# Kernel tuning notes

Hardware: AMD Instinct MI355X
Metric: run time of the kernel (lower is better)

## Reference

```python
import jax, jax.numpy as jnp
import numpy as np

BLK = 46  # hardcoded block size in the original module
EPS = 1e-5


def setup_inputs() -> dict:
    key = jax.random.key(0)
    ks = jax.random.split(key, 13)
    N, C, Ci = 128, 512, 256
    return {
        "ori_feature": jax.random.normal(ks[0], (N, C, BLK), jnp.float32),
        "bn_gamma": jax.random.uniform(ks[1], (C,), jnp.float32),
        "bn_beta": jax.random.normal(ks[2], (C,), jnp.float32),
        "bn_mean": jax.random.normal(ks[3], (C,), jnp.float32),
        "bn_var": jax.random.uniform(ks[4], (C,), jnp.float32),
        "theta_w": jax.random.normal(ks[5], (Ci, C), jnp.float32) * 0.02,
        "theta_b": jax.random.normal(ks[6], (Ci,), jnp.float32) * 0.02,
        "phi_w": jax.random.normal(ks[7], (Ci, C), jnp.float32) * 0.02,
        "phi_b": jax.random.normal(ks[8], (Ci,), jnp.float32) * 0.02,
        "g_w": jax.random.normal(ks[9], (Ci, C), jnp.float32) * 0.02,
        "g_b": jax.random.normal(ks[10], (Ci,), jnp.float32) * 0.02,
        "W_w": jax.random.normal(ks[11], (C, Ci), jnp.float32) * 0.02,
        "W_b": jax.random.normal(ks[12], (C,), jnp.float32) * 0.02,
    }


def reference(ori_feature, bn_gamma, bn_beta, bn_mean, bn_var,
              theta_w, theta_b, phi_w, phi_b, g_w, g_b, W_w, W_b):
    N, C, num = ori_feature.shape  # (N, C, 46)
    # BatchNorm1d (inference-style, per-channel) + ReLU
    inv = bn_gamma / jnp.sqrt(bn_var + EPS)
    feat = jax.nn.relu(ori_feature * inv[None, :, None]
                       + (bn_beta - bn_mean * inv)[None, :, None])
    feat = feat.transpose(0, 2, 1).reshape(N * num, C)  # (T, C)
    x_theta = feat @ theta_w.T + theta_b  # (T, Ci)
    x_phi = feat @ phi_w.T + phi_b        # (T, Ci)
    attn = x_theta @ x_phi.T              # (T, T)
    # block-diagonal masking: entries within the same 46-token block set to -1000
    blk = jnp.arange(N * num) // num
    attn = jnp.where(blk[:, None] == blk[None, :], jnp.float32(-1000.0), attn)
    f_div_C = jax.nn.softmax(attn, axis=-1)
    g_x = feat @ g_w.T + g_b              # (T, Ci)
    y = f_div_C @ g_x                     # (T, Ci)
    W_y = (y @ W_w.T + W_b).reshape(N, num, C)
    att_fea = ori_feature.transpose(0, 2, 1) + W_y  # (N, 46, C)
    return att_fea, f_div_C
```

## Files before the change

kernel.cpp:

```cpp
#include <hip/hip_runtime.h>
#include <math.h>

#define N_BATCH 128
#define C_DIM   512
#define BLKSZ   46
#define T_DIM   (N_BATCH * BLKSZ)
#define CI      256
#define EPS_BN  1e-5f
#define NCB     (T_DIM / 128)

typedef __attribute__((ext_vector_type(8))) short bf16x8;
typedef __attribute__((ext_vector_type(4))) float f32x4;

__device__ __forceinline__ short f2bf(float f) {
    union { float f; unsigned u; } v; v.f = f;
    unsigned r = v.u + 0x7fffu + ((v.u >> 16) & 1u);
    return (short)(r >> 16);
}

__device__ __forceinline__ float h2f(unsigned short h) {
    _Float16 x; __builtin_memcpy(&x, &h, 2); return (float)x;
}
__device__ __forceinline__ unsigned short f2h(float f) {
    _Float16 x = (_Float16)f; unsigned short u; __builtin_memcpy(&u, &x, 2); return u;
}

__device__ __forceinline__ void gload16(const void* g, void* l) {
    __builtin_amdgcn_global_load_lds((__attribute__((address_space(1))) void*)g,
                                     (__attribute__((address_space(3))) void*)l,
                                     16, 0, 0);
}

template <int A> struct avec_sel { using t = float4; };
template <> struct avec_sel<2> { using t = ushort4; };

__global__ __launch_bounds__(256) void bn_relu_kernel(
    const float* __restrict__ ori, const float* __restrict__ gamma,
    const float* __restrict__ beta, const float* __restrict__ mean,
    const float* __restrict__ var, short* __restrict__ feat)
{
    __shared__ short tile[256 * BLKSZ];
    const int n = blockIdx.y;
    const int c0 = blockIdx.x * 256;
    const int tid = threadIdx.x;
    for (int i = tid; i < 256 * BLKSZ; i += 256) {
        int cl = i / BLKSZ, b = i - cl * BLKSZ;
        int c = c0 + cl;
        float inv = gamma[c] * rsqrtf(var[c] + EPS_BN);
        float v = ori[((size_t)n * C_DIM + c) * BLKSZ + b] * inv + (beta[c] - mean[c] * inv);
        tile[cl * BLKSZ + b] = f2bf(fmaxf(v, 0.0f));
    }
    __syncthreads();
    for (int i = tid; i < BLKSZ * 256; i += 256) {
        int b = i >> 8, cl = i & 255;
        feat[(size_t)(n * BLKSZ + b) * C_DIM + c0 + cl] = tile[cl * BLKSZ + b];
    }
}

__global__ __launch_bounds__(256) void cvt_kernel(
    const float* __restrict__ thw, const float* __restrict__ phw,
    const float* __restrict__ gw, const float* __restrict__ Ww,
    const float* __restrict__ thb, const float* __restrict__ phb,
    const float* __restrict__ gb,
    short* __restrict__ wall, short* __restrict__ wW, float* __restrict__ bcat)
{
    const int i = blockIdx.x * 256 + threadIdx.x;
    const float* src[4] = {thw, phw, gw, Ww};
    short* dst[4] = {wall, wall + 256 * 512, wall + 512 * 512, wW};
    #pragma unroll
    for (int m = 0; m < 4; ++m) {
        float4 v = *(const float4*)(src[m] + (size_t)i * 4);
        short4 t = make_short4(f2bf(v.x), f2bf(v.y), f2bf(v.z), f2bf(v.w));
        *(short4*)(dst[m] + (size_t)i * 4) = t;
    }
    if (blockIdx.x == 0) {
        bcat[threadIdx.x] = thb[threadIdx.x];
        bcat[threadIdx.x + 256] = phb[threadIdx.x];
        bcat[threadIdx.x + 512] = gb[threadIdx.x];
    }
}

template <int EPI, int ACVT, int BM, int BN, int OCC = 2>
__global__ __launch_bounds__(256, OCC) void gemm_nt(
    const void* __restrict__ Avoid, const short* __restrict__ B,
    const float* __restrict__ bias, void* __restrict__ Cvoid,
    int M, int Nn, int K, int lda, int ldb, int nsplit,
    const float* __restrict__ ori,
    float* __restrict__ stats, const float* __restrict__ rowstat,
    float* __restrict__ fout)
{
    constexpr int NWC = BN / 64;
    constexpr int NWR = 4 / NWC;
    constexpr int MI  = BM / (NWR * 16);
    constexpr int NBUF = (ACVT != 0) ? 2 : 1;
    static_assert((EPI != 5 && EPI != 6 && EPI != 7) || NWC == 2, "stats/split epilogue assumes NWC==2");
    static_assert(ACVT == 0 || BN == 256, "pipelined vmcnt count assumes BN==256");
    __shared__ short As[NBUF * BM * 32];
    __shared__ short Bs[NBUF * BN * 32];
    const int tid = threadIdx.x;
    const int w = tid >> 6, lane = tid & 63;

    int bx = blockIdx.x, by = blockIdx.y;
    if constexpr (EPI == 5 || EPI == 6) {
        const int nwg = gridDim.x * gridDim.y;
        const int orig = by * gridDim.x + bx;
        const int q = nwg >> 3, r = nwg & 7;
        const int xcd = orig & 7, idx = orig >> 3;
        const int wg = (xcd < r ? xcd * (q + 1) : r * (q + 1) + (xcd - r) * q) + idx;
        bx = wg % gridDim.x; by = wg / gridDim.x;
    }
    const int m0 = by * BM, n0 = bx * BN;
    const int wr = w / NWC, wc = w % NWC;
    const int wrow = wr * (MI * 16);

    const int kper = K / 32 / nsplit;
    const int kt0 = blockIdx.z * kper, kt1 = kt0 + kper;

    f32x4 acc[MI][4] = {};

    const int sr = tid >> 2;
    const int sc = (tid & 3) * 8;
    const short* Ab = (const short*)Avoid;

    if constexpr (ACVT == 0) {
        for (int kt = kt0; kt < kt1; ++kt) {
            const int k0 = kt * 32;
            #pragma unroll
            for (int p = 0; p < BM / 64; ++p)
                gload16(Ab + (size_t)(m0 + p * 64 + sr) * lda + k0 + sc,
                        &As[(p * 64 + sr) * 32 + sc]);
            #pragma unroll
            for (int p = 0; p < BN / 64; ++p)
                gload16(B + (size_t)(n0 + p * 64 + sr) * ldb + k0 + sc,
                        &Bs[(p * 64 + sr) * 32 + sc]);
            __syncthreads();

            bf16x8 af[MI], bfr[4];
            #pragma unroll
            for (int i = 0; i < MI; ++i)
                af[i] = *(bf16x8*)&As[(wrow + i * 16 + (lane & 15)) * 32 + (lane >> 4) * 8];
            #pragma unroll
            for (int j = 0; j < 4; ++j)
                bfr[j] = *(bf16x8*)&Bs[(wc * 64 + j * 16 + (lane & 15)) * 32 + (lane >> 4) * 8];
            #pragma unroll
            for (int i = 0; i < MI; ++i)
                #pragma unroll
                for (int j = 0; j < 4; ++j)
                    acc[i][j] = __builtin_amdgcn_mfma_f32_16x16x32_bf16(af[i], bfr[j], acc[i][j], 0, 0, 0);
            __syncthreads();
        }
    } else {
        constexpr int EPT = BM * 32 / 256;
        static_assert(EPT == 4, "pipelined ACVT path assumes EPT==4");
        constexpr int TPR = 32 / EPT;
        const int a_r = tid / TPR;
        const int a_c = (tid % TPR) * EPT;
        float2 st = ((const float2*)rowstat)[m0 + a_r];
        const float rm = st.x, rz = st.y;
        using AV = typename avec_sel<ACVT>::t;
        const AV* Arow = (const AV*)((const char*)Avoid
                         + ((size_t)(m0 + a_r) * lda) * (ACVT == 2 ? 2 : 4));
        float* frow = fout + (size_t)(m0 + a_r) * lda;

        AV hv = Arow[(kt0 * 32 + a_c) / 4];
        #pragma unroll
        for (int p = 0; p < BN / 64; ++p)
            gload16(B + (size_t)(n0 + p * 64 + sr) * ldb + kt0 * 32 + sc,
                    &Bs[(p * 64 + sr) * 32 + sc]);

        for (int kt = kt0; kt < kt1; ++kt) {
            const int cur = (kt - kt0) & 1;
            const int kc = kt * 32 + a_c;
            float4 vf;
            if constexpr (ACVT == 2) {
                vf.x = h2f(hv.x); vf.y = h2f(hv.y); vf.z = h2f(hv.z); vf.w = h2f(hv.w);
            } else {
                vf.x = hv.x; vf.y = hv.y; vf.z = hv.z; vf.w = hv.w;
            }
            float4 e;
            e.x = expf(vf.x - rm) * rz; e.y = expf(vf.y - rm) * rz;
            e.z = expf(vf.z - rm) * rz; e.w = expf(vf.w - rm) * rz;
            *(float4*)(frow + kc) = e;
            short4 t = make_short4(f2bf(e.x), f2bf(e.y), f2bf(e.z), f2bf(e.w));
            *(short4*)&As[cur * BM * 32 + a_r * 32 + a_c] = t;

            if (kt + 1 < kt1) {
                hv = Arow[((kt + 1) * 32 + a_c) / 4];
                #pragma unroll
                for (int p = 0; p < BN / 64; ++p)
                    gload16(B + (size_t)(n0 + p * 64 + sr) * ldb + (kt + 1) * 32 + sc,
                            &Bs[(cur ^ 1) * BN * 32 + (p * 64 + sr) * 32 + sc]);
                asm volatile("s_waitcnt vmcnt(6) lgkmcnt(0)\n\ts_barrier" ::: "memory");
            } else {
                asm volatile("s_waitcnt vmcnt(1) lgkmcnt(0)\n\ts_barrier" ::: "memory");
            }

            bf16x8 af[MI], bfr[4];
            #pragma unroll
            for (int i = 0; i < MI; ++i)
                af[i] = *(bf16x8*)&As[cur * BM * 32 + (wrow + i * 16 + (lane & 15)) * 32 + (lane >> 4) * 8];
            #pragma unroll
            for (int j = 0; j < 4; ++j)
                bfr[j] = *(bf16x8*)&Bs[cur * BN * 32 + (wc * 64 + j * 16 + (lane & 15)) * 32 + (lane >> 4) * 8];
            #pragma unroll
            for (int i = 0; i < MI; ++i)
                #pragma unroll
                for (int j = 0; j < 4; ++j)
                    acc[i][j] = __builtin_amdgcn_mfma_f32_16x16x32_bf16(af[i], bfr[j], acc[i][j], 0, 0, 0);
            asm volatile("s_barrier" ::: "memory");
        }
    }

    const int col = lane & 15, rowq = lane >> 4;

    if constexpr (EPI == 5 || EPI == 6) {
        __shared__ float sm[NWC][BM];
        __shared__ float ss[NWC][BM];
        int cbj[4];
        #pragma unroll
        for (int j = 0; j < 4; ++j)
            cbj[j] = (n0 + wc * 64 + j * 16 + col) / BLKSZ;
        #pragma unroll
        for (int i = 0; i < MI; ++i) {
            #pragma unroll
            for (int r = 0; r < 4; ++r) {
                const int trow = wrow + i * 16 + rowq * 4 + r;
                const int grow = m0 + trow;
                const int rb = grow / BLKSZ;
                float vj[4];
                float vmax = -1e30f;
                #pragma unroll
                for (int j = 0; j < 4; ++j) {
                    float v = acc[i][j][r];
                    if (cbj[j] == rb) v = -30000.0f;
                    const size_t idx = (size_t)grow * Nn + (n0 + wc * 64 + j * 16 + col);
                    if constexpr (EPI == 6) {
                        unsigned short hh = f2h(v);
                        ((unsigned short*)Cvoid)[idx] = hh;
                        v = h2f(hh);
                    } else {
                        ((float*)Cvoid)[idx] = v;
                    }
                    vj[j] = v;
                    vmax = fmaxf(vmax, v);
                }
                #pragma unroll
                for (int off = 1; off < 16; off <<= 1)
                    vmax = fmaxf(vmax, __shfl_xor(vmax, off));
                float s = 0.f;
                #pragma unroll
                for (int j = 0; j < 4; ++j) s += expf(vj[j] - vmax);
                #pragma unroll
                for (int off = 1; off < 16; off <<= 1)
                    s += __shfl_xor(s, off);
                if (col == 0) { sm[wc][trow] = vmax; ss[wc][trow] = s; }
            }
        }
        __syncthreads();
        if (tid < BM) {
            const float ma = sm[0][tid], mb = sm[1][tid];
            const float mx = fmaxf(ma, mb);
            const float S = ss[0][tid] * expf(ma - mx) + ss[1][tid] * expf(mb - mx);
            ((float2*)stats)[(size_t)bx * M + (m0 + tid)] = make_float2(mx, S);
        }
    } else if constexpr (EPI == 7) {
        if (n0 < 512) {
            #pragma unroll
            for (int i = 0; i < MI; ++i)
                #pragma unroll
                for (int j = 0; j < 4; ++j)
                    #pragma unroll
                    for (int r = 0; r < 4; ++r) {
                        const int grow = m0 + wrow + i * 16 + rowq * 4 + r;
                        const int gcol = n0 + wc * 64 + j * 16 + col;
                        ((short*)Cvoid)[(size_t)grow * 512 + gcol] =
                            f2bf(acc[i][j][r] + bias[gcol]);
                    }
        } else {
            short* gxTp = (short*)stats;
            #pragma unroll
            for (int i = 0; i < MI; ++i)
                #pragma unroll
                for (int j = 0; j < 4; ++j) {
                    const int grow0 = m0 + wrow + i * 16 + rowq * 4;
                    const int gcol = n0 + wc * 64 + j * 16 + col;
                    const float bv = bias[gcol];
                    short4 t = make_short4(
                        f2bf(acc[i][j][0] + bv), f2bf(acc[i][j][1] + bv),
                        f2bf(acc[i][j][2] + bv), f2bf(acc[i][j][3] + bv));
                    *(short4*)&gxTp[(size_t)(gcol - 512) * T_DIM + grow0] = t;
                }
        }
    } else {
        #pragma unroll
        for (int i = 0; i < MI; ++i) {
            #pragma unroll
            for (int j = 0; j < 4; ++j) {
                #pragma unroll
                for (int r = 0; r < 4; ++r) {
                    const int grow = m0 + wrow + i * 16 + rowq * 4 + r;
                    const int gcol = n0 + wc * 64 + j * 16 + col;
                    const float v = acc[i][j][r];
                    if (EPI == 1) {
                        ((short*)Cvoid)[(size_t)grow * Nn + gcol] = f2bf(v + bias[gcol]);
                    } else if (EPI == 2) {
                        ((short*)Cvoid)[(size_t)grow * Nn + gcol] = f2bf(v + bias[grow]);
                    } else if (EPI == 3) {
                        ((float*)Cvoid)[(size_t)blockIdx.z * M * Nn + (size_t)grow * Nn + gcol] = v;
                    } else {
                        const int nb = grow / BLKSZ, bb = grow - nb * BLKSZ;
                        ((float*)Cvoid)[(size_t)grow * Nn + gcol] =
                            v + bias[gcol] + ori[((size_t)nb * C_DIM + gcol) * BLKSZ + bb];
                    }
                }
            }
        }
    }
}

__global__ __launch_bounds__(256) void combine_stats_kernel(
    const float* __restrict__ stats, float* __restrict__ rowstat)
{
    const int row = blockIdx.x * 256 + threadIdx.x;
    float m = -1e30f, Z = 0.f;
    for (int cb = 0; cb < NCB; ++cb) {
        float2 p = ((const float2*)stats)[(size_t)cb * T_DIM + row];
        float nm = fmaxf(m, p.x);
        Z = Z * expf(m - nm) + p.y * expf(p.x - nm);
        m = nm;
    }
    ((float2*)rowstat)[row] = make_float2(m, 1.0f / Z);
}

__global__ __launch_bounds__(256) void reduce_y_kernel(
    const float* __restrict__ part, short* __restrict__ y, int ns)
{
    const size_t i = (size_t)blockIdx.x * 256 + threadIdx.x;
    float4 s = *(const float4*)(part + i * 4);
    for (int z = 1; z < ns; ++z) {
        float4 v = *(const float4*)(part + (size_t)z * T_DIM * CI + i * 4);
        s.x += v.x; s.y += v.y; s.z += v.z; s.w += v.w;
    }
    short4 t = make_short4(f2bf(s.x), f2bf(s.y), f2bf(s.z), f2bf(s.w));
    *(short4*)(y + i * 4) = t;
}

extern "C" void kernel_launch(void* const* d_in, const int* in_sizes, int n_in,
                              void* d_out, int out_size, void* d_ws, size_t ws_size,
                              hipStream_t stream)
{
    const float* ori     = (const float*)d_in[0];
    const float* gamma   = (const float*)d_in[1];
    const float* beta    = (const float*)d_in[2];
    const float* mean    = (const float*)d_in[3];
    const float* var     = (const float*)d_in[4];
    const float* theta_w = (const float*)d_in[5];
    const float* theta_b = (const float*)d_in[6];
    const float* phi_w   = (const float*)d_in[7];
    const float* phi_b   = (const float*)d_in[8];
    const float* g_w     = (const float*)d_in[9];
    const float* g_b     = (const float*)d_in[10];
    const float* W_w     = (const float*)d_in[11];
    const float* W_b     = (const float*)d_in[12];

    float* out = (float*)d_out;
    float* P   = out + (size_t)T_DIM * C_DIM;

    char* wsb = (char*)d_ws;
    short* feat = (short*)wsb;  wsb += (size_t)T_DIM * C_DIM * 2;
    short* xcat = (short*)wsb;  wsb += (size_t)T_DIM * 512 * 2;
    short* gxT  = (short*)wsb;  wsb += (size_t)CI * T_DIM * 2;
    short* wall = (short*)wsb;  wsb += (size_t)768 * C_DIM * 2;
    short* wW   = (short*)wsb;  wsb += (size_t)C_DIM * CI * 2;
    float* bcat = (float*)wsb;  wsb += 768 * 4;
    short* ybf  = (short*)wsb;  wsb += (size_t)T_DIM * CI * 2;
    float* rowstat = (float*)wsb; wsb += (size_t)T_DIM * 8;

    const size_t base   = (size_t)(wsb - (char*)d_ws);
    const size_t p16sz  = (size_t)T_DIM * T_DIM * 2;
    const size_t ypsz4  = 4u * (size_t)T_DIM * CI * 4u;
    const bool bigws = ws_size >= base + p16sz + ypsz4;

    bn_relu_kernel<<<dim3(2, 128), 256, 0, stream>>>(ori, gamma, beta, mean, var, feat);
    cvt_kernel<<<128, 256, 0, stream>>>(theta_w, phi_w, g_w, W_w, theta_b, phi_b, g_b,
                                        wall, wW, bcat);

    gemm_nt<7, 0, 128, 128><<<dim3(6, T_DIM / 128), 256, 0, stream>>>(
        feat, wall, bcat, xcat, T_DIM, 768, C_DIM, C_DIM, C_DIM, 1, nullptr,
        (float*)gxT, nullptr, nullptr);

    if (bigws) {
        unsigned short* p16 = (unsigned short*)wsb;
        float* ypart = (float*)(wsb + p16sz);
        float* stats = ypart;

        gemm_nt<6, 0, 128, 128><<<dim3(T_DIM / 128, T_DIM / 128), 256, 0, stream>>>(
            xcat, xcat + CI, nullptr, p16, T_DIM, T_DIM, CI, 512, 512, 1, nullptr,
            stats, nullptr, nullptr);
        combine_stats_kernel<<<T_DIM / 256, 256, 0, stream>>>(stats, rowstat);
        gemm_nt<3, 2, 32, 256, 4><<<dim3(1, T_DIM / 32, 4), 256, 0, stream>>>(
            p16, gxT, nullptr, ypart, T_DIM, CI, T_DIM, T_DIM, T_DIM, 4, nullptr,
            nullptr, rowstat, P);
        reduce_y_kernel<<<(T_DIM * CI / 4) / 256, 256, 0, stream>>>(ypart, ybf, 4);
    } else {
        float* ypart = (float*)wsb;
        float* stats = ypart;
        const int ns = (ws_size >= base + ypsz4) ? 4 : 2;

        gemm_nt<5, 0, 128, 128><<<dim3(T_DIM / 128, T_DIM / 128), 256, 0, stream>>>(
            xcat, xcat + CI, nullptr, P, T_DIM, T_DIM, CI, 512, 512, 1, nullptr,
            stats, nullptr, nullptr);
        combine_stats_kernel<<<T_DIM / 256, 256, 0, stream>>>(stats, rowstat);
        gemm_nt<3, 1, 32, 256, 4><<<dim3(1, T_DIM / 32, ns), 256, 0, stream>>>(
            P, gxT, nullptr, ypart, T_DIM, CI, T_DIM, T_DIM, T_DIM, ns, nullptr,
            nullptr, rowstat, P);
        reduce_y_kernel<<<(T_DIM * CI / 4) / 256, 256, 0, stream>>>(ypart, ybf, ns);
    }

    gemm_nt<4, 0, 128, 128><<<dim3(C_DIM / 128, T_DIM / 128), 256, 0, stream>>>(
        ybf, wW, W_b, out, T_DIM, C_DIM, CI, CI, CI, 1, ori,
        nullptr, nullptr, nullptr);
}
```

Before: 340.6 us.

## Double-buffer GEMM loads, triple-buffer B in softmax-PV GEMM, store fp16 partials

The plain GEMM path gets double-buffered shared-memory staging so global loads for tile t+2 overlap the MFMA work on tile t, with hand-placed vmcnt waits. The fused softmax-times-g GEMM now prefetches two stages ahead, using triple-buffered B tiles and a two-deep register queue for A, and its occupancy hint drops from 4 to 3 to fit the larger shared-memory footprint. Split-K partial sums are stored as fp16 instead of fp32, halving partial-sum traffic, which costs precision and risks overflow or rounding error in the partial results.

```diff
diff --git a/kernel.cpp b/kernel.cpp
--- a/kernel.cpp
+++ b/kernel.cpp
@@ -92,11 +92,12 @@
     constexpr int NWC = BN / 64;
     constexpr int NWR = 4 / NWC;
     constexpr int MI  = BM / (NWR * 16);
-    constexpr int NBUF = (ACVT != 0) ? 2 : 1;
+    constexpr int NBB = (ACVT != 0) ? 3 : 2;
     static_assert((EPI != 5 && EPI != 6 && EPI != 7) || NWC == 2, "stats/split epilogue assumes NWC==2");
-    static_assert(ACVT == 0 || BN == 256, "pipelined vmcnt count assumes BN==256");
-    __shared__ short As[NBUF * BM * 32];
-    __shared__ short Bs[NBUF * BN * 32];
+    static_assert(ACVT == 0 || (BN == 256 && BM == 32), "pipelined ACVT path geometry");
+    static_assert(ACVT != 0 || (BM / 64 + BN / 64 == 4), "vmcnt(4) assumes 4 gloads/stage");
+    __shared__ short As[2 * BM * 32];
+    __shared__ short Bs[NBB * BN * 32];
     const int tid = threadIdx.x;
     const int w = tid >> 6, lane = tid & 63;
 
@@ -115,6 +116,7 @@
 
     const int kper = K / 32 / nsplit;
     const int kt0 = blockIdx.z * kper, kt1 = kt0 + kper;
+    const int ktn = kt1 - kt0;
 
     f32x4 acc[MI][4] = {};
 
@@ -123,31 +125,40 @@
     const short* Ab = (const short*)Avoid;
 
     if constexpr (ACVT == 0) {
-        for (int kt = kt0; kt < kt1; ++kt) {
+        auto stageAB = [&](int kt, int buf) {
             const int k0 = kt * 32;
             #pragma unroll
             for (int p = 0; p < BM / 64; ++p)
                 gload16(Ab + (size_t)(m0 + p * 64 + sr) * lda + k0 + sc,
-                        &As[(p * 64 + sr) * 32 + sc]);
+                        &As[buf * BM * 32 + (p * 64 + sr) * 32 + sc]);
             #pragma unroll
             for (int p = 0; p < BN / 64; ++p)
                 gload16(B + (size_t)(n0 + p * 64 + sr) * ldb + k0 + sc,
-                        &Bs[(p * 64 + sr) * 32 + sc]);
-            __syncthreads();
-
+                        &Bs[buf * BN * 32 + (p * 64 + sr) * 32 + sc]);
+        };
+        stageAB(kt0, 0);
+        if (ktn > 1) stageAB(kt0 + 1, 1);
+        if (ktn > 1) asm volatile("s_waitcnt vmcnt(4)\n\ts_barrier" ::: "memory");
+        else         asm volatile("s_waitcnt vmcnt(0)\n\ts_barrier" ::: "memory");
+
+        for (int t = 0; t < ktn; ++t) {
+            const int cur = t & 1;
             bf16x8 af[MI], bfr[4];
             #pragma unroll
             for (int i = 0; i < MI; ++i)
-                af[i] = *(bf16x8*)&As[(wrow + i * 16 + (lane & 15)) * 32 + (lane >> 4) * 8];
+                af[i] = *(bf16x8*)&As[cur * BM * 32 + (wrow + i * 16 + (lane & 15)) * 32 + (lane >> 4) * 8];
             #pragma unroll
             for (int j = 0; j < 4; ++j)
-                bfr[j] = *(bf16x8*)&Bs[(wc * 64 + j * 16 + (lane & 15)) * 32 + (lane >> 4) * 8];
+                bfr[j] = *(bf16x8*)&Bs[cur * BN * 32 + (wc * 64 + j * 16 + (lane & 15)) * 32 + (lane >> 4) * 8];
+            asm volatile("s_waitcnt lgkmcnt(0)\n\ts_barrier" ::: "memory");
+            if (t + 2 < ktn) stageAB(kt0 + t + 2, cur);
             #pragma unroll
             for (int i = 0; i < MI; ++i)
                 #pragma unroll
                 for (int j = 0; j < 4; ++j)
                     acc[i][j] = __builtin_amdgcn_mfma_f32_16x16x32_bf16(af[i], bfr[j], acc[i][j], 0, 0, 0);
-            __syncthreads();
+            if (t + 2 < ktn)      asm volatile("s_waitcnt vmcnt(4)\n\ts_barrier" ::: "memory");
+            else if (t + 1 < ktn) asm volatile("s_waitcnt vmcnt(0)\n\ts_barrier" ::: "memory");
         }
     } else {
         constexpr int EPT = BM * 32 / 256;
@@ -162,52 +173,60 @@
                          + ((size_t)(m0 + a_r) * lda) * (ACVT == 2 ? 2 : 4));
         float* frow = fout + (size_t)(m0 + a_r) * lda;
 
-        AV hv = Arow[(kt0 * 32 + a_c) / 4];
-        #pragma unroll
-        for (int p = 0; p < BN / 64; ++p)
-            gload16(B + (size_t)(n0 + p * 64 + sr) * ldb + kt0 * 32 + sc,
-                    &Bs[(p * 64 + sr) * 32 + sc]);
-
-        for (int kt = kt0; kt < kt1; ++kt) {
-            const int cur = (kt - kt0) & 1;
-            const int kc = kt * 32 + a_c;
+        auto stageB = [&](int kt, int buf) {
+            #pragma unroll
+            for (int p = 0; p < BN / 64; ++p)
+                gload16(B + (size_t)(n0 + p * 64 + sr) * ldb + kt * 32 + sc,
+                        &Bs[buf * BN * 32 + (p * 64 + sr) * 32 + sc]);
+        };
+
+        AV hva = Arow[(kt0 * 32 + a_c) / 4];
+        AV hvb = hva;
+        stageB(kt0, 0);
+        if (ktn > 1) { hvb = Arow[((kt0 + 1) * 32 + a_c) / 4]; stageB(kt0 + 1, 1); }
+        if (ktn > 1) asm volatile("s_waitcnt vmcnt(4)" ::: "memory");
+        else         asm volatile("s_waitcnt vmcnt(0)" ::: "memory");
+
+        int curB = 0, stB = 2;
+        for (int t = 0; t < ktn; ++t) {
+            const int kt = kt0 + t;
+            const int curA = t & 1;
+            AV v = hva; hva = hvb;
             float4 vf;
             if constexpr (ACVT == 2) {
-                vf.x = h2f(hv.x); vf.y = h2f(hv.y); vf.z = h2f(hv.z); vf.w = h2f(hv.w);
+                vf.x = h2f(v.x); vf.y = h2f(v.y); vf.z = h2f(v.z); vf.w = h2f(v.w);
             } else {
-                vf.x = hv.x; vf.y = hv.y; vf.z = hv.z; vf.w = hv.w;
+                vf.x = v.x; vf.y = v.y; vf.z = v.z; vf.w = v.w;
             }
             float4 e;
             e.x = expf(vf.x - rm) * rz; e.y = expf(vf.y - rm) * rz;
             e.z = expf(vf.z - rm) * rz; e.w = expf(vf.w - rm) * rz;
-            *(float4*)(frow + kc) = e;
-            short4 t = make_short4(f2bf(e.x), f2bf(e.y), f2bf(e.z), f2bf(e.w));
-            *(short4*)&As[cur * BM * 32 + a_r * 32 + a_c] = t;
-
-            if (kt + 1 < kt1) {
-                hv = Arow[((kt + 1) * 32 + a_c) / 4];
-                #pragma unroll
-                for (int p = 0; p < BN / 64; ++p)
-                    gload16(B + (size_t)(n0 + p * 64 + sr) * ldb + (kt + 1) * 32 + sc,
-                            &Bs[(cur ^ 1) * BN * 32 + (p * 64 + sr) * 32 + sc]);
-                asm volatile("s_waitcnt vmcnt(6) lgkmcnt(0)\n\ts_barrier" ::: "memory");
-            } else {
-                asm volatile("s_waitcnt vmcnt(1) lgkmcnt(0)\n\ts_barrier" ::: "memory");
-            }
+            *(float4*)(frow + kt * 32 + a_c) = e;
+            short4 tq = make_short4(f2bf(e.x), f2bf(e.y), f2bf(e.z), f2bf(e.w));
+            *(short4*)&As[curA * BM * 32 + a_r * 32 + a_c] = tq;
+            if (t + 2 < ktn) hvb = Arow[((kt + 2) * 32 + a_c) / 4];
+
+            asm volatile("s_waitcnt lgkmcnt(0)\n\ts_barrier" ::: "memory");
+            if (t + 2 < ktn) stageB(kt + 2, stB);
 
             bf16x8 af[MI], bfr[4];
             #pragma unroll
             for (int i = 0; i < MI; ++i)
-                af[i] = *(bf16x8*)&As[cur * BM * 32 + (wrow + i * 16 + (lane & 15)) * 32 + (lane >> 4) * 8];
+                af[i] = *(bf16x8*)&As[curA * BM * 32 + (wrow + i * 16 + (lane & 15)) * 32 + (lane >> 4) * 8];
             #pragma unroll
             for (int j = 0; j < 4; ++j)
-                bfr[j] = *(bf16x8*)&Bs[cur * BN * 32 + (wc * 64 + j * 16 + (lane & 15)) * 32 + (lane >> 4) * 8];
+                bfr[j] = *(bf16x8*)&Bs[curB * BN * 32 + (wc * 64 + j * 16 + (lane & 15)) * 32 + (lane >> 4) * 8];
             #pragma unroll
             for (int i = 0; i < MI; ++i)
                 #pragma unroll
                 for (int j = 0; j < 4; ++j)
                     acc[i][j] = __builtin_amdgcn_mfma_f32_16x16x32_bf16(af[i], bfr[j], acc[i][j], 0, 0, 0);
-            asm volatile("s_barrier" ::: "memory");
+
+            if (t + 2 < ktn)      asm volatile("s_waitcnt vmcnt(6)\n\ts_barrier" ::: "memory");
+            else if (t + 1 < ktn) asm volatile("s_waitcnt vmcnt(1)\n\ts_barrier" ::: "memory");
+            else                  asm volatile("s_waitcnt vmcnt(0)\n\ts_barrier" ::: "memory");
+            curB = (curB == 2) ? 0 : curB + 1;
+            stB  = (stB == 2) ? 0 : stB + 1;
         }
     }
 
@@ -306,7 +325,7 @@
                     } else if (EPI == 2) {
                         ((short*)Cvoid)[(size_t)grow * Nn + gcol] = f2bf(v + bias[grow]);
                     } else if (EPI == 3) {
-                        ((float*)Cvoid)[(size_t)blockIdx.z * M * Nn + (size_t)grow * Nn + gcol] = v;
+                        ((unsigned short*)Cvoid)[(size_t)blockIdx.z * M * Nn + (size_t)grow * Nn + gcol] = f2h(v);
                     } else {
                         const int nb = grow / BLKSZ, bb = grow - nb * BLKSZ;
                         ((float*)Cvoid)[(size_t)grow * Nn + gcol] =
@@ -333,15 +352,15 @@
 }
 
 __global__ __launch_bounds__(256) void reduce_y_kernel(
-    const float* __restrict__ part, short* __restrict__ y, int ns)
+    const unsigned short* __restrict__ part, short* __restrict__ y, int ns)
 {
     const size_t i = (size_t)blockIdx.x * 256 + threadIdx.x;
-    float4 s = *(const float4*)(part + i * 4);
-    for (int z = 1; z < ns; ++z) {
-        float4 v = *(const float4*)(part + (size_t)z * T_DIM * CI + i * 4);
-        s.x += v.x; s.y += v.y; s.z += v.z; s.w += v.w;
-    }
-    short4 t = make_short4(f2bf(s.x), f2bf(s.y), f2bf(s.z), f2bf(s.w));
+    float s0 = 0.f, s1 = 0.f, s2 = 0.f, s3 = 0.f;
+    for (int z = 0; z < ns; ++z) {
+        ushort4 v = *(const ushort4*)(part + (size_t)z * T_DIM * CI + i * 4);
+        s0 += h2f(v.x); s1 += h2f(v.y); s2 += h2f(v.z); s3 += h2f(v.w);
+    }
+    short4 t = make_short4(f2bf(s0), f2bf(s1), f2bf(s2), f2bf(s3));
     *(short4*)(y + i * 4) = t;
 }
 
@@ -378,7 +397,7 @@
 
     const size_t base   = (size_t)(wsb - (char*)d_ws);
     const size_t p16sz  = (size_t)T_DIM * T_DIM * 2;
-    const size_t ypsz4  = 4u * (size_t)T_DIM * CI * 4u;
+    const size_t ypsz4  = 4u * (size_t)T_DIM * CI * 2u;
     const bool bigws = ws_size >= base + p16sz + ypsz4;
 
     bn_relu_kernel<<<dim3(2, 128), 256, 0, stream>>>(ori, gamma, beta, mean, var, feat);
@@ -391,27 +410,27 @@
 
     if (bigws) {
         unsigned short* p16 = (unsigned short*)wsb;
-        float* ypart = (float*)(wsb + p16sz);
-        float* stats = ypart;
+        unsigned short* ypart = (unsigned short*)(wsb + p16sz);
+        float* stats = (float*)ypart;
 
         gemm_nt<6, 0, 128, 128><<<dim3(T_DIM / 128, T_DIM / 128), 256, 0, stream>>>(
             xcat, xcat + CI, nullptr, p16, T_DIM, T_DIM, CI, 512, 512, 1, nullptr,
             stats, nullptr, nullptr);
         combine_stats_kernel<<<T_DIM / 256, 256, 0, stream>>>(stats, rowstat);
-        gemm_nt<3, 2, 32, 256, 4><<<dim3(1, T_DIM / 32, 4), 256, 0, stream>>>(
+        gemm_nt<3, 2, 32, 256, 3><<<dim3(1, T_DIM / 32, 4), 256, 0, stream>>>(
             p16, gxT, nullptr, ypart, T_DIM, CI, T_DIM, T_DIM, T_DIM, 4, nullptr,
             nullptr, rowstat, P);
         reduce_y_kernel<<<(T_DIM * CI / 4) / 256, 256, 0, stream>>>(ypart, ybf, 4);
     } else {
-        float* ypart = (float*)wsb;
-        float* stats = ypart;
+        unsigned short* ypart = (unsigned short*)wsb;
+        float* stats = (float*)wsb;
         const int ns = (ws_size >= base + ypsz4) ? 4 : 2;
 
         gemm_nt<5, 0, 128, 128><<<dim3(T_DIM / 128, T_DIM / 128), 256, 0, stream>>>(
             xcat, xcat + CI, nullptr, P, T_DIM, T_DIM, CI, 512, 512, 1, nullptr,
             stats, nullptr, nullptr);
         combine_stats_kernel<<<T_DIM / 256, 256, 0, stream>>>(stats, rowstat);
-        gemm_nt<3, 1, 32, 256, 4><<<dim3(1, T_DIM / 32, ns), 256, 0, stream>>>(
+        gemm_nt<3, 1, 32, 256, 3><<<dim3(1, T_DIM / 32, ns), 256, 0, stream>>>(
             P, gxT, nullptr, ypart, T_DIM, CI, T_DIM, T_DIM, T_DIM, ns, nullptr,
             nullptr, rowstat, P);
         reduce_y_kernel<<<(T_DIM * CI / 4) / 256, 256, 0, stream>>>(ypart, ybf, ns);
```

Result: faster. 331.2 us (-2.8%).
